# Kernel optimization log

Hardware: AMD Instinct MI355X
Metric: run time of the kernel (lower is better)

The kernel has to match this reference:

```python
import jax, jax.numpy as jnp
import numpy as np

N = 8_000_000  # number of (parent, child, relation) edges
N_RELS = 64
P = 3  # n_polarities


def sparsemax(z):
    # sparsemax along last axis (Martins & Astudillo 2016)
    d = z.shape[-1]
    zs = jnp.sort(z, axis=-1)[..., ::-1]          # descending
    cs = jnp.cumsum(zs, axis=-1)
    k = jnp.arange(1, d + 1, dtype=z.dtype)
    support = 1.0 + k * zs > cs                   # [.., d] bool
    ksup = jnp.sum(support, axis=-1, keepdims=True)  # int, size of support
    tau = (jnp.take_along_axis(cs, ksup - 1, axis=-1) - 1.0) / ksup.astype(z.dtype)
    return jnp.maximum(z - tau, 0.0)


def setup_inputs() -> dict:
    key = jax.random.key(0)
    k1, k2, k3, k4, k5 = jax.random.split(key, 5)
    prnt_probs = jax.random.uniform(k1, (N, P), dtype=jnp.float32)
    child_probs = jax.random.uniform(k2, (N, P), dtype=jnp.float32)
    rels = jax.random.randint(k3, (N,), 0, N_RELS, dtype=jnp.int32)
    # learned params (torch inits to ones/constants; perturb so grads are non-degenerate)
    M = 1.0 + 0.1 * jax.random.normal(k4, (N_RELS, P, P), dtype=jnp.float32)
    beta = jax.random.uniform(k5, (N_RELS, P), dtype=jnp.float32)
    z_epsilon = jnp.float32(0.01)
    scale_factor = jnp.float32(21.0)
    return {"prnt_probs": prnt_probs, "child_probs": child_probs, "M": M,
            "beta": beta, "z_epsilon": z_epsilon, "scale_factor": scale_factor,
            "rels": rels, "var_sfx": 0}


def reference(prnt_probs, child_probs, M, beta, z_epsilon, scale_factor, rels, var_sfx):
    # All rows of child_probs/prnt_probs are nonzero (uniform fill), so the
    # nonzero() gathers select every edge and the copy branch is empty:
    # this is the dense alpha path of AlphaModel.forward.
    c = jnp.einsum('nij,nj->ni', M[rels], child_probs)  # relation-gated bmm
    c = sparsemax(c)
    c = sparsemax(c)  # alpha branch re-applies sparsemax (idempotent but faithful)
    p = sparsemax(prnt_probs)
    b = beta[rels]
    alpha = (1.0 - b) * p + b * c
    # scale(): entropy of clamped mixture + cosine similarity
    z = jnp.maximum(p + c, jax.lax.stop_gradient(z_epsilon))  # torch uses .item() -> no grad
    z = z / jnp.sum(z, axis=-1, keepdims=True)
    entropy = -jnp.sum(z * jnp.log(z), axis=-1)
    cos = jnp.sum(p * c, axis=-1)
    norm = jnp.maximum(jnp.linalg.norm(p, axis=-1) * jnp.linalg.norm(c, axis=-1), 1e-10)
    cos = 0.1 + cos / norm
    scale = scale_factor * cos / entropy
    alpha = jnp.maximum(alpha * scale[:, None], 0.001)
    return alpha
```

## Files before the change

kernel.cpp:

```cpp
#include <hip/hip_runtime.h>

#define BLOCK 256
#define NWAVES (BLOCK / 64)

typedef float f32x4 __attribute__((ext_vector_type(4)));

__device__ __forceinline__ float fast_ln(float x) {
    return 0.69314718056f * __builtin_amdgcn_logf(x);
}
__device__ __forceinline__ float fast_rcp(float x) {
    return __builtin_amdgcn_rcpf(x);
}
__device__ __forceinline__ float fast_rsq(float x) {
    return __builtin_amdgcn_rsqf(x);
}

__device__ __forceinline__ float bperm(int ab, float v) {
    return __int_as_float(__builtin_amdgcn_ds_bpermute(ab, __float_as_int(v)));
}

__device__ __forceinline__ void gload_lds16(const float* g, float* l) {
    __builtin_amdgcn_global_load_lds(
        (const __attribute__((address_space(1))) unsigned int*)g,
        (__attribute__((address_space(3))) unsigned int*)l,
        16, 0, 0);
}

__device__ __forceinline__ void sparsemax3(float z0, float z1, float z2,
                                           float& o0, float& o1, float& o2) {
    float lo01 = fminf(z0, z1), hi01 = fmaxf(z0, z1);
    float s2 = fminf(lo01, z2);
    float mx = fmaxf(lo01, z2);
    float s0 = fmaxf(hi01, mx);
    float s1 = fminf(hi01, mx);
    float cs2 = s0 + s1;
    float cs3 = cs2 + s2;
    bool k2 = (1.0f + 2.0f * s1 > cs2);
    bool k3 = (1.0f + 3.0f * s2 > cs3);
    int k = 1 + (int)k2 + (int)k3;
    float csk = (k == 1) ? s0 : ((k == 2) ? cs2 : cs3);
    float rk  = (k == 1) ? 1.0f : ((k == 2) ? 0.5f : 0.33333334f);
    float tau = (csk - 1.0f) * rk;
    o0 = fmaxf(z0 - tau, 0.0f);
    o1 = fmaxf(z1 - tau, 0.0f);
    o2 = fmaxf(z2 - tau, 0.0f);
}

__device__ __forceinline__ void edge_core(
    float p0, float p1, float p2,
    float q0, float q1, float q2,
    float m00, float m01, float m02,
    float m10, float m11, float m12,
    float m20, float m21, float m22,
    float b0, float b1, float b2,
    float zeps, float sf,
    float& a0o, float& a1o, float& a2o)
{
    float c0 = m00 * q0 + m01 * q1 + m02 * q2;
    float c1 = m10 * q0 + m11 * q1 + m12 * q2;
    float c2 = m20 * q0 + m21 * q1 + m22 * q2;
    sparsemax3(c0, c1, c2, c0, c1, c2);
    sparsemax3(p0, p1, p2, p0, p1, p2);
    float a0 = p0 + b0 * (c0 - p0);
    float a1 = p1 + b1 * (c1 - p1);
    float a2 = p2 + b2 * (c2 - p2);
    float z0 = fmaxf(p0 + c0, zeps);
    float z1 = fmaxf(p1 + c1, zeps);
    float z2 = fmaxf(p2 + c2, zeps);
    float rs = fast_rcp(z0 + z1 + z2);
    z0 *= rs; z1 *= rs; z2 *= rs;
    float ent = -(z0 * fast_ln(z0) + z1 * fast_ln(z1) + z2 * fast_ln(z2));
    float dot = p0 * c0 + p1 * c1 + p2 * c2;
    float pp = p0 * p0 + p1 * p1 + p2 * p2;
    float cc = c0 * c0 + c1 * c1 + c2 * c2;
    float cosv = 0.1f + dot * fast_rsq(fmaxf(pp * cc, 1e-20f));
    float scale = sf * cosv * fast_rcp(ent);
    a0o = fmaxf(a0 * scale, 0.001f);
    a1o = fmaxf(a1 * scale, 0.001f);
    a2o = fmaxf(a2 * scale, 0.001f);
}

__global__ __launch_bounds__(BLOCK, 6) void alpha_kernel(
    const float* __restrict__ prnt, const float* __restrict__ child,
    const float* __restrict__ Mg, const float* __restrict__ betag,
    const float* __restrict__ zeps_p, const float* __restrict__ sf_p,
    const int* __restrict__ rels, float* __restrict__ out, int n_edges)
{
    __shared__ __align__(16) float sP[NWAVES * 768];
    __shared__ __align__(16) float sC[NWAVES * 768];

    const int tid  = threadIdx.x;
    const int lane = tid & 63;
    const int w    = tid >> 6;

    float mt[9], bt[3];
    {
        const float* mr = Mg + lane * 9;
#pragma unroll
        for (int k = 0; k < 9; ++k) mt[k] = mr[k];
        const float* br = betag + lane * 3;
#pragma unroll
        for (int k = 0; k < 3; ++k) bt[k] = br[k];
    }

    const float zeps = zeps_p[0];
    const float sf   = sf_p[0];
    const int nt4 = n_edges >> 2;
    const int t = blockIdx.x * BLOCK + tid;

    if (nt4 > 0) {
        const int NT4F = 3 * nt4;
        const int WB   = 3 * (blockIdx.x * BLOCK + (w << 6));
        float* lp = &sP[w * 768];
        float* lc = &sC[w * 768];

#pragma unroll
        for (int j = 0; j < 3; ++j) {
            int g = min(WB + j * 64 + lane, NT4F - 1);
            gload_lds16(prnt  + 4 * g, lp + j * 256);
            gload_lds16(child + 4 * g, lc + j * 256);
        }
        int4 r4 = ((const int4*)rels)[min(t, nt4 - 1)];

        asm volatile("s_waitcnt vmcnt(0)" ::: "memory");

        f32x4 pa = *(const f32x4*)(lp + lane * 12);
        f32x4 pb = *(const f32x4*)(lp + lane * 12 + 4);
        f32x4 pc = *(const f32x4*)(lp + lane * 12 + 8);
        f32x4 ca = *(const f32x4*)(lc + lane * 12);
        f32x4 cb = *(const f32x4*)(lc + lane * 12 + 4);
        f32x4 cc = *(const f32x4*)(lc + lane * 12 + 8);

        float P[12] = {pa.x, pa.y, pa.z, pa.w, pb.x, pb.y, pb.z, pb.w,
                       pc.x, pc.y, pc.z, pc.w};
        float C[12] = {ca.x, ca.y, ca.z, ca.w, cb.x, cb.y, cb.z, cb.w,
                       cc.x, cc.y, cc.z, cc.w};
        int R[4] = {r4.x, r4.y, r4.z, r4.w};
        float O[12];
#pragma unroll
        for (int e = 0; e < 4; ++e) {
            int ab = R[e] << 2;
            float g0 = bperm(ab, mt[0]), g1 = bperm(ab, mt[1]), g2 = bperm(ab, mt[2]);
            float g3 = bperm(ab, mt[3]), g4 = bperm(ab, mt[4]), g5 = bperm(ab, mt[5]);
            float g6 = bperm(ab, mt[6]), g7 = bperm(ab, mt[7]), g8 = bperm(ab, mt[8]);
            float h0 = bperm(ab, bt[0]), h1 = bperm(ab, bt[1]), h2 = bperm(ab, bt[2]);
            edge_core(P[3 * e], P[3 * e + 1], P[3 * e + 2],
                      C[3 * e], C[3 * e + 1], C[3 * e + 2],
                      g0, g1, g2, g3, g4, g5, g6, g7, g8,
                      h0, h1, h2, zeps, sf,
                      O[3 * e], O[3 * e + 1], O[3 * e + 2]);
        }

        *(f32x4*)(lp + lane * 12)     = f32x4{O[0], O[1], O[2],  O[3]};
        *(f32x4*)(lp + lane * 12 + 4) = f32x4{O[4], O[5], O[6],  O[7]};
        *(f32x4*)(lp + lane * 12 + 8) = f32x4{O[8], O[9], O[10], O[11]};
        asm volatile("s_waitcnt lgkmcnt(0)" ::: "memory");

#pragma unroll
        for (int j = 0; j < 3; ++j) {
            int g = WB + j * 64 + lane;
            if (g < NT4F) {
                f32x4 v = *(const f32x4*)(lp + j * 256 + lane * 4);
                *(f32x4*)(out + 4 * g) = v;
            }
        }
    }

    if (blockIdx.x == 0 && threadIdx.x == 0) {
        for (int e = (n_edges >> 2) * 4; e < n_edges; ++e) {
            int r = rels[e];
            const float* m = Mg + r * 9;
            const float* b = betag + r * 3;
            float a0, a1, a2;
            edge_core(prnt[3 * e], prnt[3 * e + 1], prnt[3 * e + 2],
                      child[3 * e], child[3 * e + 1], child[3 * e + 2],
                      m[0], m[1], m[2], m[3], m[4], m[5], m[6], m[7], m[8],
                      b[0], b[1], b[2], zeps, sf, a0, a1, a2);
            out[3 * e] = a0; out[3 * e + 1] = a1; out[3 * e + 2] = a2;
        }
    }
}

extern "C" void kernel_launch(void* const* d_in, const int* in_sizes, int n_in,
                              void* d_out, int out_size, void* d_ws, size_t ws_size,
                              hipStream_t stream) {
    const float* prnt  = (const float*)d_in[0];
    const float* child = (const float*)d_in[1];
    const float* Mg    = (const float*)d_in[2];
    const float* betag = (const float*)d_in[3];
    const float* zeps  = (const float*)d_in[4];
    const float* sf    = (const float*)d_in[5];
    const int*   rels  = (const int*)d_in[6];
    float* out = (float*)d_out;

    int n_edges = in_sizes[0] / 3;
    int nt4 = n_edges >> 2;
    int nblocks = (nt4 + BLOCK - 1) / BLOCK;
    if (nblocks < 1) nblocks = 1;
    alpha_kernel<<<nblocks, BLOCK, 0, stream>>>(
        prnt, child, Mg, betag, zeps, sf, rels, out, n_edges);
}
```

Before: 263.5 us.

## Use a persistent grid with double-buffered LDS prefetch of edge data

The one-tile-per-block launch becomes a fixed grid of 768 blocks that loop over edge tiles with a grid stride. While the current tile is computed, the next tile's prnt and child data go into a second LDS buffer via global_load_lds, and its rels are prefetched into registers, synchronised with a partial vmcnt wait. The aim is to hide global-load latency and cut block launch overhead. In exchange, the launch-bound occupancy hint drops from 6 to 3 blocks and LDS use doubles, so fewer waves are resident to hide latency.

```diff
diff --git a/kernel.cpp b/kernel.cpp
--- a/kernel.cpp
+++ b/kernel.cpp
@@ -2,6 +2,7 @@
 
 #define BLOCK 256
 #define NWAVES (BLOCK / 64)
+#define GRID 768
 
 typedef float f32x4 __attribute__((ext_vector_type(4)));
 
@@ -80,14 +81,14 @@
     a2o = fmaxf(a2 * scale, 0.001f);
 }
 
-__global__ __launch_bounds__(BLOCK, 6) void alpha_kernel(
+__global__ __launch_bounds__(BLOCK, 3) void alpha_kernel(
     const float* __restrict__ prnt, const float* __restrict__ child,
     const float* __restrict__ Mg, const float* __restrict__ betag,
     const float* __restrict__ zeps_p, const float* __restrict__ sf_p,
     const int* __restrict__ rels, float* __restrict__ out, int n_edges)
 {
-    __shared__ __align__(16) float sP[NWAVES * 768];
-    __shared__ __align__(16) float sC[NWAVES * 768];
+    __shared__ __align__(16) float sP[2][NWAVES * 768];
+    __shared__ __align__(16) float sC[2][NWAVES * 768];
 
     const int tid  = threadIdx.x;
     const int lane = tid & 63;
@@ -106,63 +107,85 @@
     const float zeps = zeps_p[0];
     const float sf   = sf_p[0];
     const int nt4 = n_edges >> 2;
-    const int t = blockIdx.x * BLOCK + tid;
 
     if (nt4 > 0) {
         const int NT4F = 3 * nt4;
-        const int WB   = 3 * (blockIdx.x * BLOCK + (w << 6));
-        float* lp = &sP[w * 768];
-        float* lc = &sC[w * 768];
-
-#pragma unroll
-        for (int j = 0; j < 3; ++j) {
-            int g = min(WB + j * 64 + lane, NT4F - 1);
-            gload_lds16(prnt  + 4 * g, lp + j * 256);
-            gload_lds16(child + 4 * g, lc + j * 256);
-        }
-        int4 r4 = ((const int4*)rels)[min(t, nt4 - 1)];
-
-        asm volatile("s_waitcnt vmcnt(0)" ::: "memory");
-
-        f32x4 pa = *(const f32x4*)(lp + lane * 12);
-        f32x4 pb = *(const f32x4*)(lp + lane * 12 + 4);
-        f32x4 pc = *(const f32x4*)(lp + lane * 12 + 8);
-        f32x4 ca = *(const f32x4*)(lc + lane * 12);
-        f32x4 cb = *(const f32x4*)(lc + lane * 12 + 4);
-        f32x4 cc = *(const f32x4*)(lc + lane * 12 + 8);
-
-        float P[12] = {pa.x, pa.y, pa.z, pa.w, pb.x, pb.y, pb.z, pb.w,
-                       pc.x, pc.y, pc.z, pc.w};
-        float C[12] = {ca.x, ca.y, ca.z, ca.w, cb.x, cb.y, cb.z, cb.w,
-                       cc.x, cc.y, cc.z, cc.w};
-        int R[4] = {r4.x, r4.y, r4.z, r4.w};
-        float O[12];
-#pragma unroll
-        for (int e = 0; e < 4; ++e) {
-            int ab = R[e] << 2;
-            float g0 = bperm(ab, mt[0]), g1 = bperm(ab, mt[1]), g2 = bperm(ab, mt[2]);
-            float g3 = bperm(ab, mt[3]), g4 = bperm(ab, mt[4]), g5 = bperm(ab, mt[5]);
-            float g6 = bperm(ab, mt[6]), g7 = bperm(ab, mt[7]), g8 = bperm(ab, mt[8]);
-            float h0 = bperm(ab, bt[0]), h1 = bperm(ab, bt[1]), h2 = bperm(ab, bt[2]);
-            edge_core(P[3 * e], P[3 * e + 1], P[3 * e + 2],
-                      C[3 * e], C[3 * e + 1], C[3 * e + 2],
-                      g0, g1, g2, g3, g4, g5, g6, g7, g8,
-                      h0, h1, h2, zeps, sf,
-                      O[3 * e], O[3 * e + 1], O[3 * e + 2]);
-        }
-
-        *(f32x4*)(lp + lane * 12)     = f32x4{O[0], O[1], O[2],  O[3]};
-        *(f32x4*)(lp + lane * 12 + 4) = f32x4{O[4], O[5], O[6],  O[7]};
-        *(f32x4*)(lp + lane * 12 + 8) = f32x4{O[8], O[9], O[10], O[11]};
-        asm volatile("s_waitcnt lgkmcnt(0)" ::: "memory");
-
-#pragma unroll
-        for (int j = 0; j < 3; ++j) {
-            int g = WB + j * 64 + lane;
-            if (g < NT4F) {
-                f32x4 v = *(const f32x4*)(lp + j * 256 + lane * 4);
-                *(f32x4*)(out + 4 * g) = v;
-            }
+        const int S    = GRID * BLOCK;
+        const int t0   = blockIdx.x * BLOCK + tid;
+        const int wt0  = blockIdx.x * BLOCK + (w << 6);
+        const int iters = (nt4 + S - 1) / S;
+
+        auto stage = [&](int k, int b) {
+            const int base3 = 3 * (wt0 + k * S);
+            float* lp = &sP[b][w * 768];
+            float* lc = &sC[b][w * 768];
+#pragma unroll
+            for (int j = 0; j < 3; ++j) {
+                int g = min(base3 + j * 64 + lane, NT4F - 1);
+                gload_lds16(prnt  + 4 * g, lp + j * 256);
+                gload_lds16(child + 4 * g, lc + j * 256);
+            }
+        };
+
+        int4 rnext = ((const int4*)rels)[min(t0, nt4 - 1)];
+        stage(0, 0);
+
+        int cur = 0;
+        for (int k = 0; k < iters; ++k) {
+            const int4 rcur = rnext;
+            const bool more = (k + 1 < iters);
+            if (more) {
+                rnext = ((const int4*)rels)[min(t0 + (k + 1) * S, nt4 - 1)];
+                stage(k + 1, cur ^ 1);
+            }
+            if (more) asm volatile("s_waitcnt vmcnt(7)" ::: "memory");
+            else      asm volatile("s_waitcnt vmcnt(0)" ::: "memory");
+
+            float* lp = &sP[cur][w * 768];
+            float* lc = &sC[cur][w * 768];
+
+            f32x4 pa = *(const f32x4*)(lp + lane * 12);
+            f32x4 pb = *(const f32x4*)(lp + lane * 12 + 4);
+            f32x4 pc = *(const f32x4*)(lp + lane * 12 + 8);
+            f32x4 ca = *(const f32x4*)(lc + lane * 12);
+            f32x4 cb = *(const f32x4*)(lc + lane * 12 + 4);
+            f32x4 cc = *(const f32x4*)(lc + lane * 12 + 8);
+
+            float P[12] = {pa.x, pa.y, pa.z, pa.w, pb.x, pb.y, pb.z, pb.w,
+                           pc.x, pc.y, pc.z, pc.w};
+            float C[12] = {ca.x, ca.y, ca.z, ca.w, cb.x, cb.y, cb.z, cb.w,
+                           cc.x, cc.y, cc.z, cc.w};
+            int R[4] = {rcur.x, rcur.y, rcur.z, rcur.w};
+            float O[12];
+#pragma unroll
+            for (int e = 0; e < 4; ++e) {
+                int ab = R[e] << 2;
+                float g0 = bperm(ab, mt[0]), g1 = bperm(ab, mt[1]), g2 = bperm(ab, mt[2]);
+                float g3 = bperm(ab, mt[3]), g4 = bperm(ab, mt[4]), g5 = bperm(ab, mt[5]);
+                float g6 = bperm(ab, mt[6]), g7 = bperm(ab, mt[7]), g8 = bperm(ab, mt[8]);
+                float h0 = bperm(ab, bt[0]), h1 = bperm(ab, bt[1]), h2 = bperm(ab, bt[2]);
+                edge_core(P[3 * e], P[3 * e + 1], P[3 * e + 2],
+                          C[3 * e], C[3 * e + 1], C[3 * e + 2],
+                          g0, g1, g2, g3, g4, g5, g6, g7, g8,
+                          h0, h1, h2, zeps, sf,
+                          O[3 * e], O[3 * e + 1], O[3 * e + 2]);
+            }
+
+            *(f32x4*)(lp + lane * 12)     = f32x4{O[0], O[1], O[2],  O[3]};
+            *(f32x4*)(lp + lane * 12 + 4) = f32x4{O[4], O[5], O[6],  O[7]};
+            *(f32x4*)(lp + lane * 12 + 8) = f32x4{O[8], O[9], O[10], O[11]};
+            asm volatile("s_waitcnt lgkmcnt(0)" ::: "memory");
+
+            const int base3 = 3 * (wt0 + k * S);
+#pragma unroll
+            for (int j = 0; j < 3; ++j) {
+                int g = base3 + j * 64 + lane;
+                if (g < NT4F) {
+                    f32x4 v = *(const f32x4*)(lp + j * 256 + lane * 4);
+                    *(f32x4*)(out + 4 * g) = v;
+                }
+            }
+            cur ^= 1;
         }
     }
 
@@ -194,9 +217,6 @@
     float* out = (float*)d_out;
 
     int n_edges = in_sizes[0] / 3;
-    int nt4 = n_edges >> 2;
-    int nblocks = (nt4 + BLOCK - 1) / BLOCK;
-    if (nblocks < 1) nblocks = 1;
-    alpha_kernel<<<nblocks, BLOCK, 0, stream>>>(
+    alpha_kernel<<<GRID, BLOCK, 0, stream>>>(
         prnt, child, Mg, betag, zeps, sf, rels, out, n_edges);
 }
```

Result: slower. 272.1 us (+3.3%).

## Process two quads of edges per thread with a direct-register second half

Applied to the files above, without the earlier changes.

Each thread now handles 8 edges: the first quad is staged through LDS via global_load_lds as before, and the second quad (from the upper half of the array) is loaded directly into registers with vector loads and written straight to global memory. This halves the grid and raises memory-level parallelism per thread, overlapping compute of one quad with the other's loads. Launch bounds drop from 6 to 4 blocks per CU, which allows more registers at the cost of occupancy. The second quad's direct stores are 48-byte strided per lane, so they are less coalesced than the LDS-staged path.

```diff
diff --git a/kernel.cpp b/kernel.cpp
--- a/kernel.cpp
+++ b/kernel.cpp
@@ -80,7 +80,7 @@
     a2o = fmaxf(a2 * scale, 0.001f);
 }
 
-__global__ __launch_bounds__(BLOCK, 6) void alpha_kernel(
+__global__ __launch_bounds__(BLOCK, 4) void alpha_kernel(
     const float* __restrict__ prnt, const float* __restrict__ child,
     const float* __restrict__ Mg, const float* __restrict__ betag,
     const float* __restrict__ zeps_p, const float* __restrict__ sf_p,
@@ -105,24 +105,62 @@
 
     const float zeps = zeps_p[0];
     const float sf   = sf_p[0];
-    const int nt4 = n_edges >> 2;
-    const int t = blockIdx.x * BLOCK + tid;
-
-    if (nt4 > 0) {
-        const int NT4F = 3 * nt4;
-        const int WB   = 3 * (blockIdx.x * BLOCK + (w << 6));
+    const int nQ = n_edges >> 2;
+    const int nT = nQ >> 1;
+
+    if (nT > 0) {
+        const int t   = blockIdx.x * BLOCK + tid;
+        const int tc  = min(t, nT - 1);
+        const int wt0 = blockIdx.x * BLOCK + (w << 6);
+        const int F1  = 3 * nT;
+        const int qd  = tc + nT;
+
         float* lp = &sP[w * 768];
         float* lc = &sC[w * 768];
 
+        const int4* r4p = (const int4*)rels;
+        int4 ra = r4p[tc];
+        int4 rd = r4p[qd];
 #pragma unroll
         for (int j = 0; j < 3; ++j) {
-            int g = min(WB + j * 64 + lane, NT4F - 1);
+            int g = min(3 * wt0 + j * 64 + lane, F1 - 1);
             gload_lds16(prnt  + 4 * g, lp + j * 256);
             gload_lds16(child + 4 * g, lc + j * 256);
         }
-        int4 r4 = ((const int4*)rels)[min(t, nt4 - 1)];
+        const f32x4* p4 = (const f32x4*)prnt;
+        const f32x4* c4 = (const f32x4*)child;
+        f32x4 dpa = p4[3 * qd], dpb = p4[3 * qd + 1], dpc = p4[3 * qd + 2];
+        f32x4 dca = c4[3 * qd], dcb = c4[3 * qd + 1], dcc = c4[3 * qd + 2];
 
         asm volatile("s_waitcnt vmcnt(0)" ::: "memory");
+
+        {
+            float P[12] = {dpa.x, dpa.y, dpa.z, dpa.w, dpb.x, dpb.y, dpb.z,
+                           dpb.w, dpc.x, dpc.y, dpc.z, dpc.w};
+            float C[12] = {dca.x, dca.y, dca.z, dca.w, dcb.x, dcb.y, dcb.z,
+                           dcb.w, dcc.x, dcc.y, dcc.z, dcc.w};
+            int R[4] = {rd.x, rd.y, rd.z, rd.w};
+            float O[12];
+#pragma unroll
+            for (int e = 0; e < 4; ++e) {
+                int ab = R[e] << 2;
+                float g0 = bperm(ab, mt[0]), g1 = bperm(ab, mt[1]), g2 = bperm(ab, mt[2]);
+                float g3 = bperm(ab, mt[3]), g4 = bperm(ab, mt[4]), g5 = bperm(ab, mt[5]);
+                float g6 = bperm(ab, mt[6]), g7 = bperm(ab, mt[7]), g8 = bperm(ab, mt[8]);
+                float h0 = bperm(ab, bt[0]), h1 = bperm(ab, bt[1]), h2 = bperm(ab, bt[2]);
+                edge_core(P[3 * e], P[3 * e + 1], P[3 * e + 2],
+                          C[3 * e], C[3 * e + 1], C[3 * e + 2],
+                          g0, g1, g2, g3, g4, g5, g6, g7, g8,
+                          h0, h1, h2, zeps, sf,
+                          O[3 * e], O[3 * e + 1], O[3 * e + 2]);
+            }
+            if (t < nT) {
+                f32x4* o4 = (f32x4*)out;
+                o4[3 * qd]     = f32x4{O[0], O[1], O[2],  O[3]};
+                o4[3 * qd + 1] = f32x4{O[4], O[5], O[6],  O[7]};
+                o4[3 * qd + 2] = f32x4{O[8], O[9], O[10], O[11]};
+            }
+        }
 
         f32x4 pa = *(const f32x4*)(lp + lane * 12);
         f32x4 pb = *(const f32x4*)(lp + lane * 12 + 4);
@@ -130,36 +168,36 @@
         f32x4 ca = *(const f32x4*)(lc + lane * 12);
         f32x4 cb = *(const f32x4*)(lc + lane * 12 + 4);
         f32x4 cc = *(const f32x4*)(lc + lane * 12 + 8);
-
-        float P[12] = {pa.x, pa.y, pa.z, pa.w, pb.x, pb.y, pb.z, pb.w,
-                       pc.x, pc.y, pc.z, pc.w};
-        float C[12] = {ca.x, ca.y, ca.z, ca.w, cb.x, cb.y, cb.z, cb.w,
-                       cc.x, cc.y, cc.z, cc.w};
-        int R[4] = {r4.x, r4.y, r4.z, r4.w};
-        float O[12];
-#pragma unroll
-        for (int e = 0; e < 4; ++e) {
-            int ab = R[e] << 2;
-            float g0 = bperm(ab, mt[0]), g1 = bperm(ab, mt[1]), g2 = bperm(ab, mt[2]);
-            float g3 = bperm(ab, mt[3]), g4 = bperm(ab, mt[4]), g5 = bperm(ab, mt[5]);
-            float g6 = bperm(ab, mt[6]), g7 = bperm(ab, mt[7]), g8 = bperm(ab, mt[8]);
-            float h0 = bperm(ab, bt[0]), h1 = bperm(ab, bt[1]), h2 = bperm(ab, bt[2]);
-            edge_core(P[3 * e], P[3 * e + 1], P[3 * e + 2],
-                      C[3 * e], C[3 * e + 1], C[3 * e + 2],
-                      g0, g1, g2, g3, g4, g5, g6, g7, g8,
-                      h0, h1, h2, zeps, sf,
-                      O[3 * e], O[3 * e + 1], O[3 * e + 2]);
-        }
-
-        *(f32x4*)(lp + lane * 12)     = f32x4{O[0], O[1], O[2],  O[3]};
-        *(f32x4*)(lp + lane * 12 + 4) = f32x4{O[4], O[5], O[6],  O[7]};
-        *(f32x4*)(lp + lane * 12 + 8) = f32x4{O[8], O[9], O[10], O[11]};
+        {
+            float P[12] = {pa.x, pa.y, pa.z, pa.w, pb.x, pb.y, pb.z, pb.w,
+                           pc.x, pc.y, pc.z, pc.w};
+            float C[12] = {ca.x, ca.y, ca.z, ca.w, cb.x, cb.y, cb.z, cb.w,
+                           cc.x, cc.y, cc.z, cc.w};
+            int R[4] = {ra.x, ra.y, ra.z, ra.w};
+            float O[12];
+#pragma unroll
+            for (int e = 0; e < 4; ++e) {
+                int ab = R[e] << 2;
+                float g0 = bperm(ab, mt[0]), g1 = bperm(ab, mt[1]), g2 = bperm(ab, mt[2]);
+                float g3 = bperm(ab, mt[3]), g4 = bperm(ab, mt[4]), g5 = bperm(ab, mt[5]);
+                float g6 = bperm(ab, mt[6]), g7 = bperm(ab, mt[7]), g8 = bperm(ab, mt[8]);
+                float h0 = bperm(ab, bt[0]), h1 = bperm(ab, bt[1]), h2 = bperm(ab, bt[2]);
+                edge_core(P[3 * e], P[3 * e + 1], P[3 * e + 2],
+                          C[3 * e], C[3 * e + 1], C[3 * e + 2],
+                          g0, g1, g2, g3, g4, g5, g6, g7, g8,
+                          h0, h1, h2, zeps, sf,
+                          O[3 * e], O[3 * e + 1], O[3 * e + 2]);
+            }
+            *(f32x4*)(lp + lane * 12)     = f32x4{O[0], O[1], O[2],  O[3]};
+            *(f32x4*)(lp + lane * 12 + 4) = f32x4{O[4], O[5], O[6],  O[7]};
+            *(f32x4*)(lp + lane * 12 + 8) = f32x4{O[8], O[9], O[10], O[11]};
+        }
         asm volatile("s_waitcnt lgkmcnt(0)" ::: "memory");
 
 #pragma unroll
         for (int j = 0; j < 3; ++j) {
-            int g = WB + j * 64 + lane;
-            if (g < NT4F) {
+            int g = 3 * wt0 + j * 64 + lane;
+            if (g < F1) {
                 f32x4 v = *(const f32x4*)(lp + j * 256 + lane * 4);
                 *(f32x4*)(out + 4 * g) = v;
             }
@@ -167,7 +205,7 @@
     }
 
     if (blockIdx.x == 0 && threadIdx.x == 0) {
-        for (int e = (n_edges >> 2) * 4; e < n_edges; ++e) {
+        for (int e = (n_edges >> 3) * 8; e < n_edges; ++e) {
             int r = rels[e];
             const float* m = Mg + r * 9;
             const float* b = betag + r * 3;
@@ -194,8 +232,8 @@
     float* out = (float*)d_out;
 
     int n_edges = in_sizes[0] / 3;
-    int nt4 = n_edges >> 2;
-    int nblocks = (nt4 + BLOCK - 1) / BLOCK;
+    int nT = n_edges >> 3;
+    int nblocks = (nT + BLOCK - 1) / BLOCK;
     if (nblocks < 1) nblocks = 1;
     alpha_kernel<<<nblocks, BLOCK, 0, stream>>>(
         prnt, child, Mg, betag, zeps, sf, rels, out, n_edges);
```

Measured after the change: 264.8 us. Within noise of the previous version (+0.5%).
